# Optimization experiments

Measured on AMD Instinct MI355X. Metric: run time of the kernel, lower is better.

Reference implementation:

```python
import jax, jax.numpy as jnp
import numpy as np

N = 50000      # nodes
E = 600000     # edges
H = 128        # hidden_features (= in_features)
ED = 16        # edge_attr_dim
B = 256        # number of graphs in batch
L = 5          # num_layers
OUT = 128      # out_features


def _xavier(key, shape):
    fan_in, fan_out = shape
    a = float(np.sqrt(6.0 / (fan_in + fan_out)))
    return jax.random.uniform(key, shape, jnp.float32, -a, a)


def setup_inputs() -> dict:
    key = jax.random.key(0)
    ks = jax.random.split(key, 32)
    x = jax.random.normal(ks[0], (N, H), jnp.float32)
    edge_index = jax.random.randint(ks[1], (2, E), 0, N, jnp.int32)
    edge_attr = jax.random.normal(ks[2], (E, ED), jnp.float32)
    batch = jnp.sort(jax.random.randint(ks[3], (N,), 0, B, jnp.int32))
    # per-layer parameters, stacked along leading L axis (in=hidden so uniform)
    node_W = jnp.stack([_xavier(jax.random.fold_in(ks[4], i), (H, H)) for i in range(L)])
    edge_W = jnp.stack([_xavier(jax.random.fold_in(ks[5], i), (ED, H)) for i in range(L)])
    mlp1_W = jnp.stack([_xavier(jax.random.fold_in(ks[6], i), (H, H)) for i in range(L)])
    mlp2_W = jnp.stack([_xavier(jax.random.fold_in(ks[7], i), (H, H)) for i in range(L)])
    zb = jnp.zeros((L, H), jnp.float32)
    # virtual-node update MLP (shared across layers) and final classifier
    vn_w0 = _xavier(ks[8], (H, H)); vn_b0 = jnp.zeros((H,), jnp.float32)
    vn_w1 = _xavier(ks[9], (H, H)); vn_b1 = jnp.zeros((H,), jnp.float32)
    fc_W = _xavier(ks[10], (H, OUT)); fc_b = jnp.zeros((OUT,), jnp.float32)
    vn_init = jnp.zeros((1, H), jnp.float32)  # embedding initialized to 0
    return {
        "x": x, "edge_attr": edge_attr,
        "node_W": node_W, "node_b": zb, "edge_W": edge_W, "edge_b": zb,
        "mlp1_W": mlp1_W, "mlp1_b": zb, "mlp2_W": mlp2_W, "mlp2_b": zb,
        "vn_w0": vn_w0, "vn_b0": vn_b0, "vn_w1": vn_w1, "vn_b1": vn_b1,
        "fc_W": fc_W, "fc_b": fc_b, "vn_init": vn_init,
        "edge_index": edge_index, "batch": batch,
    }


def reference(x, edge_attr, node_W, node_b, edge_W, edge_b, mlp1_W, mlp1_b,
              mlp2_W, mlp2_b, vn_w0, vn_b0, vn_w1, vn_b1, fc_W, fc_b,
              vn_init, edge_index, batch):
    src, dst = edge_index[0], edge_index[1]
    # per-graph node counts for mean pooling (guard against empty graphs)
    counts = jnp.maximum(
        jax.ops.segment_sum(jnp.ones((N, 1), x.dtype), batch, num_segments=B), 1.0)
    vn = jnp.broadcast_to(vn_init, (B, H))  # weight.repeat(batch_size, 1)

    def layer(carry, p):
        xc, vn = carry
        nW, nb, eW, eb, m1W, m1b, m2W, m2b = p
        h = xc @ nW + nb + vn[batch]              # node encode + VN broadcast
        ea = edge_attr @ eW + eb                   # edge encode [E,H]
        msg = h[src] + ea                          # gather + add
        agg = jax.ops.segment_sum(msg, dst, num_segments=N)  # scatter-add
        out = jax.nn.relu(agg @ m1W + m1b) @ m2W + m2b        # layer MLP
        xn = jax.nn.relu(out)
        pooled = jax.ops.segment_sum(xn, batch, num_segments=B) / counts
        vn2 = vn + jax.nn.relu(jax.nn.relu(pooled @ vn_w0 + vn_b0) @ vn_w1 + vn_b1)
        return (xn, vn2), None

    (xf, _), _ = jax.lax.scan(
        layer, (x, vn),
        (node_W, node_b, edge_W, edge_b, mlp1_W, mlp1_b, mlp2_W, mlp2_b))
    pooled = jax.ops.segment_sum(xf, batch, num_segments=B) / counts
    return pooled @ fc_W + fc_b
```

## Files before the change

### kernel.cpp

```cpp
#include <hip/hip_runtime.h>

#define NN 50000
#define EE 600000
#define HH 128
#define EDD 16
#define BB 256
#define LL 5
#define NN16 (NN * 16)
#define NSHADOW 8

typedef float f32x4 __attribute__((ext_vector_type(4)));
typedef _Float16 f16x4 __attribute__((ext_vector_type(4)));
typedef _Float16 f16x8 __attribute__((ext_vector_type(8)));

__global__ __launch_bounds__(256) void wprep_k(const float* __restrict__ W,
    _Float16* __restrict__ Wh, _Float16* __restrict__ Wl, int total)
{
    int idx = blockIdx.x * 256 + threadIdx.x;
    if (idx >= total) return;
    int mat = idx >> 14;
    int r = idx & 16383;
    int j = r & 7, lane = (r >> 3) & 63, ks = (r >> 9) & 3, ntw = (r >> 11) & 7;
    int lm = lane & 15, quad = lane >> 4;
    int n = (ntw >> 1) * 32 + (ntw & 1) * 16 + lm;
    int k = ks * 32 + quad * 8 + j;
    float w = W[(mat << 14) + (k << 7) + n];
    _Float16 h = (_Float16)w;
    Wh[idx] = h;
    Wl[idx] = (_Float16)(w - (float)h);
}

__global__ __launch_bounds__(256) void xprep_k(const float* __restrict__ x,
    _Float16* __restrict__ X)
{
    int i = blockIdx.x * 256 + threadIdx.x;
    if (i >= NN * 32) return;
    float4 v = ((const float4*)x)[i];
    f16x4 o;
    o[0] = (_Float16)v.x; o[1] = (_Float16)v.y; o[2] = (_Float16)v.z; o[3] = (_Float16)v.w;
    ((f16x4*)X)[i] = o;
}

__device__ __forceinline__ void stage_A16(const _Float16* __restrict__ Ag, int M, int brow,
    int tid, _Float16* __restrict__ As)
{
    const int r = tid >> 2, cg = tid & 3;
    const int grow = brow + r;
    _Float16* p = As + r * 136 + cg * 32;
    if (grow < M) {
        const f16x8* s = (const f16x8*)(Ag + (size_t)grow * 128 + cg * 32);
#pragma unroll
        for (int i = 0; i < 4; ++i) ((f16x8*)p)[i] = s[i];
    } else {
        f16x8 z = (f16x8)(_Float16)0;
#pragma unroll
        for (int i = 0; i < 4; ++i) ((f16x8*)p)[i] = z;
    }
}

__device__ __forceinline__ void mfma_stage16(
    const _Float16* __restrict__ As,
    const _Float16* __restrict__ Wh, const _Float16* __restrict__ Wl,
    int wn, int lm, int quad, int lane, f32x4 acc[4][2])
{
    f16x8 Bh[2][4], Bl[2][4];
#pragma unroll
    for (int nt = 0; nt < 2; ++nt)
#pragma unroll
        for (int ks = 0; ks < 4; ++ks) {
            int fi = ((((wn * 2 + nt) * 4) + ks) * 64 + lane) * 8;
            Bh[nt][ks] = *(const f16x8*)(Wh + fi);
            Bl[nt][ks] = *(const f16x8*)(Wl + fi);
        }
#pragma unroll
    for (int ks = 0; ks < 4; ++ks) {
        f16x8 a[4];
#pragma unroll
        for (int mt = 0; mt < 4; ++mt) {
            int off = (mt * 16 + lm) * 136 + ks * 32 + quad * 8;
            a[mt] = *(const f16x8*)(As + off);
        }
#pragma unroll
        for (int mt = 0; mt < 4; ++mt)
#pragma unroll
            for (int nt = 0; nt < 2; ++nt) {
                acc[mt][nt] = __builtin_amdgcn_mfma_f32_16x16x32_f16(a[mt], Bh[nt][ks], acc[mt][nt], 0, 0, 0);
                acc[mt][nt] = __builtin_amdgcn_mfma_f32_16x16x32_f16(a[mt], Bl[nt][ks], acc[mt][nt], 0, 0, 0);
            }
    }
}

__device__ __forceinline__ void store_f16(const _Float16* __restrict__ Fo,
    _Float16* __restrict__ out, int M, int brow, int tid)
{
    const int r = tid >> 2, cg = tid & 3;
    const int grow = brow + r;
    if (grow >= M) return;
    const f16x8* src = (const f16x8*)(Fo + r * 136 + cg * 32);
    f16x8* dst = (f16x8*)(out + (size_t)grow * 128 + cg * 32);
#pragma unroll
    for (int i = 0; i < 4; ++i) dst[i] = src[i];
}

__global__ __launch_bounds__(256) void gemm_fused_k(
    const _Float16* __restrict__ AggX, const _Float16* __restrict__ Extra,
    const _Float16* __restrict__ WNh, const _Float16* __restrict__ WNl,
    const _Float16* __restrict__ W1h, const _Float16* __restrict__ W1l, const float* __restrict__ b1,
    const _Float16* __restrict__ W2h, const _Float16* __restrict__ W2l, const float* __restrict__ b2,
    _Float16* __restrict__ X, float* __restrict__ pooled8,
    const int* __restrict__ batch, int M)
{
    __shared__ __align__(16) _Float16 bufA[64 * 136];
    __shared__ __align__(16) _Float16 bufB[64 * 136];
    const int tid = threadIdx.x, brow = blockIdx.x * 64;

    stage_A16(AggX, M, brow, tid, bufA);
    stage_A16(Extra, M, brow, tid, bufB);
    __syncthreads();

    const int lane = tid & 63, wn = tid >> 6, lm = lane & 15, quad = lane >> 4;
    const int colb = wn * 32 + lm;

    f32x4 acc[4][2];
#pragma unroll
    for (int mt = 0; mt < 4; ++mt) { acc[mt][0] = (f32x4)(0.f); acc[mt][1] = (f32x4)(0.f); }
    mfma_stage16(bufA, WNh, WNl, wn, lm, quad, lane, acc);

#pragma unroll
    for (int mt = 0; mt < 4; ++mt) {
#pragma unroll
        for (int r = 0; r < 4; ++r) {
            int trow = mt * 16 + quad * 4 + r;
            _Float16* p0 = &bufB[trow * 136 + colb];
            _Float16* p1 = &bufB[trow * 136 + colb + 16];
            *p0 = (_Float16)(acc[mt][0][r] + (float)*p0);
            *p1 = (_Float16)(acc[mt][1][r] + (float)*p1);
        }
    }
    __syncthreads();

#pragma unroll
    for (int mt = 0; mt < 4; ++mt) { acc[mt][0] = (f32x4)(0.f); acc[mt][1] = (f32x4)(0.f); }
    mfma_stage16(bufB, W1h, W1l, wn, lm, quad, lane, acc);
    {
        const float c0 = b1[colb], c1 = b1[colb + 16];
#pragma unroll
        for (int mt = 0; mt < 4; ++mt) {
#pragma unroll
            for (int r = 0; r < 4; ++r) {
                int trow = mt * 16 + quad * 4 + r;
                bufA[trow * 136 + colb]      = (_Float16)fmaxf(acc[mt][0][r] + c0, 0.f);
                bufA[trow * 136 + colb + 16] = (_Float16)fmaxf(acc[mt][1][r] + c1, 0.f);
            }
        }
    }
    __syncthreads();

#pragma unroll
    for (int mt = 0; mt < 4; ++mt) { acc[mt][0] = (f32x4)(0.f); acc[mt][1] = (f32x4)(0.f); }
    mfma_stage16(bufA, W2h, W2l, wn, lm, quad, lane, acc);
    {
        const float d0 = b2[colb], d1 = b2[colb + 16];
#pragma unroll
        for (int mt = 0; mt < 4; ++mt) {
#pragma unroll
            for (int r = 0; r < 4; ++r) {
                int trow = mt * 16 + quad * 4 + r;
                bufB[trow * 136 + colb]      = (_Float16)fmaxf(acc[mt][0][r] + d0, 0.f);
                bufB[trow * 136 + colb + 16] = (_Float16)fmaxf(acc[mt][1][r] + d1, 0.f);
            }
        }
    }
    __syncthreads();
    store_f16(bufB, X, M, brow, tid);

    {
        float* pooled = pooled8 + (size_t)(blockIdx.x & (NSHADOW - 1)) * (BB * HH);
        const int c = tid & 127, half = tid >> 7;
        const int row0 = half * 32;
        float sum = 0.f;
        int curg = -1;
        for (int r2 = 0; r2 < 32; ++r2) {
            int grow = brow + row0 + r2;
            if (grow >= M) break;
            int g = batch[grow];
            if (g != curg) {
                if (curg >= 0) atomicAdd(&pooled[curg * 128 + c], sum);
                curg = g; sum = 0.f;
            }
            sum += (float)bufB[(row0 + r2) * 136 + c];
        }
        if (curg >= 0) atomicAdd(&pooled[curg * 128 + c], sum);
    }
}

__global__ __launch_bounds__(256) void aggregate2_k(
    const _Float16* __restrict__ X, const float* __restrict__ aggE,
    const float* __restrict__ eW, const float* __restrict__ eb, const float* __restrict__ nb,
    const _Float16* __restrict__ vn16, int usevn,
    const int* __restrict__ rowstart, const int4* __restrict__ csr,
    _Float16* __restrict__ AggX, _Float16* __restrict__ Extra, int n)
{
    __shared__ float eWs[16 * 128];
    __shared__ float cbs[128];
    const int tid = threadIdx.x;
#pragma unroll
    for (int t = 0; t < 2; ++t) {
        int li = (tid + t * 256) * 4;
        *(float4*)(&eWs[li]) = *(const float4*)(eW + li);
    }
    if (tid < 32) {
        float4 e4 = *(const float4*)(eb + tid * 4);
        float4 n4 = *(const float4*)(nb + tid * 4);
        e4.x += n4.x; e4.y += n4.y; e4.z += n4.z; e4.w += n4.w;
        *(float4*)(&cbs[tid * 4]) = e4;
    }
    __syncthreads();

    const int lane = tid & 15;
    const int node = blockIdx.x * 16 + (tid >> 4);
    if (node >= n) return;
    const int s = rowstart[node], e = rowstart[node + 1];
    const f16x8* X8 = (const f16x8*)X;
    const f16x8* V8 = (const f16x8*)vn16;

    float ax[8], ev[8];
#pragma unroll
    for (int k = 0; k < 8; ++k) { ax[k] = 0.f; ev[k] = 0.f; }

    int p = s;
    for (; p + 4 <= e; p += 4) {
        int4 c0 = csr[p], c1 = csr[p + 1], c2 = csr[p + 2], c3 = csr[p + 3];
        f16x8 x0 = X8[(size_t)c0.x * 16 + lane];
        f16x8 x1 = X8[(size_t)c1.x * 16 + lane];
        f16x8 x2 = X8[(size_t)c2.x * 16 + lane];
        f16x8 x3 = X8[(size_t)c3.x * 16 + lane];
#pragma unroll
        for (int k = 0; k < 8; ++k)
            ax[k] += ((float)x0[k] + (float)x1[k]) + ((float)x2[k] + (float)x3[k]);
        if (usevn) {
            f16x8 v0 = V8[c0.z * 16 + lane];
            f16x8 v1 = V8[c1.z * 16 + lane];
            f16x8 v2 = V8[c2.z * 16 + lane];
            f16x8 v3 = V8[c3.z * 16 + lane];
#pragma unroll
            for (int k = 0; k < 8; ++k)
                ev[k] += ((float)v0[k] + (float)v1[k]) + ((float)v2[k] + (float)v3[k]);
        }
    }
    for (; p < e; ++p) {
        int4 c0 = csr[p];
        f16x8 x0 = X8[(size_t)c0.x * 16 + lane];
#pragma unroll
        for (int k = 0; k < 8; ++k) ax[k] += (float)x0[k];
        if (usevn) {
            f16x8 v0 = V8[c0.z * 16 + lane];
#pragma unroll
            for (int k = 0; k < 8; ++k) ev[k] += (float)v0[k];
        }
    }

    const float degf = (float)(e - s);
    const float* ae = aggE + (size_t)node * 16;
    float et[8];
#pragma unroll
    for (int k = 0; k < 8; ++k) et[k] = ev[k] + degf * cbs[lane * 8 + k];
#pragma unroll
    for (int k = 0; k < 16; ++k) {
        float a = ae[k];
        float4 wa = *(const float4*)(&eWs[k * 128 + lane * 8]);
        float4 wb = *(const float4*)(&eWs[k * 128 + lane * 8 + 4]);
        et[0] = fmaf(a, wa.x, et[0]); et[1] = fmaf(a, wa.y, et[1]);
        et[2] = fmaf(a, wa.z, et[2]); et[3] = fmaf(a, wa.w, et[3]);
        et[4] = fmaf(a, wb.x, et[4]); et[5] = fmaf(a, wb.y, et[5]);
        et[6] = fmaf(a, wb.z, et[6]); et[7] = fmaf(a, wb.w, et[7]);
    }

    f16x8 ox, oe;
#pragma unroll
    for (int k = 0; k < 8; ++k) { ox[k] = (_Float16)ax[k]; oe[k] = (_Float16)et[k]; }
    ((f16x8*)AggX)[(size_t)node * 16 + lane] = ox;
    ((f16x8*)Extra)[(size_t)node * 16 + lane] = oe;
}

__global__ __launch_bounds__(256) void aggE_k(
    const float* __restrict__ eattr, const int* __restrict__ rowstart,
    const int4* __restrict__ csr, float* __restrict__ aggE, int n)
{
    const int lane = threadIdx.x & 15;
    const int node = blockIdx.x * 16 + (threadIdx.x >> 4);
    if (node >= n) return;
    const int s = rowstart[node], e = rowstart[node + 1];
    float acc = 0.f;
    for (int p = s; p < e; ++p)
        acc += eattr[(size_t)csr[p].y * 16 + lane];
    aggE[(size_t)node * 16 + lane] = acc;
}

__global__ __launch_bounds__(128) void vn_update_k(
    float* __restrict__ pooled8, const int* __restrict__ gstart,
    const float* __restrict__ W0, const float* __restrict__ b0,
    const float* __restrict__ W1, const float* __restrict__ b1,
    float* __restrict__ vn, _Float16* __restrict__ vn16)
{
    __shared__ float p[128], q[128];
    const int g = blockIdx.x, t = threadIdx.x;
    float cnt = (float)(gstart[g + 1] - gstart[g]);
    if (cnt < 1.f) cnt = 1.f;
    float sum = 0.f;
#pragma unroll
    for (int s = 0; s < NSHADOW; ++s) {
        float* slot = pooled8 + (size_t)s * (BB * HH) + g * 128 + t;
        sum += *slot;
        *slot = 0.f;
    }
    p[t] = sum / cnt;
    __syncthreads();
    float a0 = b0[t];
    for (int k = 0; k < 128; ++k) a0 = fmaf(p[k], W0[k * 128 + t], a0);
    q[t] = fmaxf(a0, 0.f);
    __syncthreads();
    float a1 = b1[t];
    for (int k = 0; k < 128; ++k) a1 = fmaf(q[k], W1[k * 128 + t], a1);
    float nv = vn[g * 128 + t] + fmaxf(a1, 0.f);
    vn[g * 128 + t] = nv;
    vn16[g * 128 + t] = (_Float16)nv;
}

__global__ __launch_bounds__(128) void fc_k(
    const float* __restrict__ pooled8, const int* __restrict__ gstart,
    const float* __restrict__ W, const float* __restrict__ b,
    float* __restrict__ out)
{
    __shared__ float p[128];
    const int g = blockIdx.x, t = threadIdx.x;
    float cnt = (float)(gstart[g + 1] - gstart[g]);
    if (cnt < 1.f) cnt = 1.f;
    float sum = 0.f;
#pragma unroll
    for (int s = 0; s < NSHADOW; ++s)
        sum += pooled8[(size_t)s * (BB * HH) + g * 128 + t];
    p[t] = sum / cnt;
    __syncthreads();
    float acc = b[t];
    for (int k = 0; k < 128; ++k) acc = fmaf(p[k], W[k * 128 + t], acc);
    out[g * 128 + t] = acc;
}

__global__ void histp_k(const int* __restrict__ idx, int n, int* __restrict__ cntp)
{
    int i = blockIdx.x * 256 + threadIdx.x;
    if (i < n) atomicAdd(&cntp[(blockIdx.x & 3) * NN16 + (idx[i] << 4)], 1);
}

__global__ void scan_deg_k(const int* __restrict__ degp, int n, int* __restrict__ out, int* __restrict__ bsum)
{
    __shared__ int s[256];
    int gid = blockIdx.x * 256 + threadIdx.x;
    int v = 0;
    if (gid < n) {
        int o = gid << 4;
        v = degp[o] + degp[NN16 + o] + degp[2 * NN16 + o] + degp[3 * NN16 + o];
    }
    s[threadIdx.x] = v;
    __syncthreads();
    for (int off = 1; off < 256; off <<= 1) {
        int t = (threadIdx.x >= off) ? s[threadIdx.x - off] : 0;
        __syncthreads();
        s[threadIdx.x] += t;
        __syncthreads();
    }
    int incl = s[threadIdx.x];
    if (gid < n) out[gid] = incl - v;
    if (bsum != nullptr && threadIdx.x == 255) bsum[blockIdx.x] = incl;
}

__global__ void scan_k(const int* __restrict__ in, int n, int* __restrict__ out, int* __restrict__ bsum)
{
    __shared__ int s[256];
    int gid = blockIdx.x * 256 + threadIdx.x;
    int v = (gid < n) ? in[gid] : 0;
    s[threadIdx.x] = v;
    __syncthreads();
    for (int off = 1; off < 256; off <<= 1) {
        int t = (threadIdx.x >= off) ? s[threadIdx.x - off] : 0;
        __syncthreads();
        s[threadIdx.x] += t;
        __syncthreads();
    }
    int incl = s[threadIdx.x];
    if (gid < n) out[gid] = incl - v;
    if (bsum != nullptr && threadIdx.x == 255) bsum[blockIdx.x] = incl;
}

__global__ void addoff_k(int* __restrict__ data, const int* __restrict__ boff, int n, int total)
{
    int i = blockIdx.x * 256 + threadIdx.x;
    if (i < n) data[i] += boff[blockIdx.x];
    if (i == 0) data[n] = total;
}

__global__ void curinit_k(const int* __restrict__ rowstart, int* __restrict__ cursorp)
{
    int i = blockIdx.x * 256 + threadIdx.x;
    if (i < NN) cursorp[i << 4] = rowstart[i];
}

__global__ void fill_k(const int* __restrict__ dst, const int* __restrict__ src, int n,
                       const int* __restrict__ batch,
                       int* __restrict__ cursorp, int4* __restrict__ csr)
{
    int e = blockIdx.x * 256 + threadIdx.x;
    if (e < n) {
        int sv = src[e];
        int slot = atomicAdd(&cursorp[dst[e] << 4], 1);
        int4 pr; pr.x = sv; pr.y = e; pr.z = batch[sv]; pr.w = 0;
        csr[slot] = pr;
    }
}

__global__ void gstart_k(const int* __restrict__ batch, int* __restrict__ gstart)
{
    int b = blockIdx.x * 64 + threadIdx.x;
    if (b > BB) return;
    if (b == BB) { gstart[BB] = NN; return; }
    int lo = 0, hi = NN;
    while (lo < hi) {
        int mid = (lo + hi) >> 1;
        if (batch[mid] < b) lo = mid + 1; else hi = mid;
    }
    gstart[b] = lo;
}

__global__ void vninit_k(const float* __restrict__ vninit, float* __restrict__ vn,
                         _Float16* __restrict__ vn16, float* __restrict__ pooled8)
{
    int i = blockIdx.x * 256 + threadIdx.x;
    if (i < BB * HH) {
        float v = vninit[i & 127];
        vn[i] = v;
        vn16[i] = (_Float16)v;
    }
    if (i < NSHADOW * BB * HH) pooled8[i] = 0.f;
}

extern "C" void kernel_launch(void* const* d_in, const int* in_sizes, int n_in,
                              void* d_out, int out_size, void* d_ws, size_t ws_size,
                              hipStream_t stream)
{
    (void)in_sizes; (void)n_in; (void)out_size; (void)ws_size;
    const float* x       = (const float*)d_in[0];
    const float* eattr   = (const float*)d_in[1];
    const float* node_W  = (const float*)d_in[2];
    const float* node_b  = (const float*)d_in[3];
    const float* edge_W  = (const float*)d_in[4];
    const float* edge_b  = (const float*)d_in[5];
    const float* mlp1_W  = (const float*)d_in[6];
    const float* mlp1_b  = (const float*)d_in[7];
    const float* mlp2_W  = (const float*)d_in[8];
    const float* mlp2_b  = (const float*)d_in[9];
    const float* vn_w0   = (const float*)d_in[10];
    const float* vn_b0   = (const float*)d_in[11];
    const float* vn_w1   = (const float*)d_in[12];
    const float* vn_b1   = (const float*)d_in[13];
    const float* fc_W    = (const float*)d_in[14];
    const float* fc_b    = (const float*)d_in[15];
    const float* vn_init = (const float*)d_in[16];
    const int*   eidx    = (const int*)d_in[17];
    const int*   batch   = (const int*)d_in[18];
    const int* srcv = eidx;
    const int* dstv = eidx + EE;

    char* wp = (char*)d_ws;
    auto alloc = [&](size_t bytes) -> void* {
        void* p = (void*)wp;
        wp += (bytes + 255) & ~(size_t)255;
        return p;
    };
    _Float16* X0   = (_Float16*)alloc((size_t)NN * HH * 2);
    _Float16* X    = (_Float16*)alloc((size_t)NN * HH * 2);
    _Float16* AggX = (_Float16*)alloc((size_t)NN * HH * 2);
    _Float16* Extra= (_Float16*)alloc((size_t)NN * HH * 2);
    float* aggE    = (float*)alloc((size_t)NN * EDD * 4);
    float* vn      = (float*)alloc((size_t)BB * HH * 4);
    _Float16* vn16 = (_Float16*)alloc((size_t)BB * HH * 2);
    float* pooled8 = (float*)alloc((size_t)NSHADOW * BB * HH * 4);
    int* degp      = (int*)alloc((size_t)4 * NN16 * 4);
    int* rowstart  = (int*)alloc((size_t)(NN + 1) * 4);
    int* cursorp   = (int*)alloc((size_t)NN16 * 4);
    int4* csr      = (int4*)alloc((size_t)EE * 16);
    int* bsum      = (int*)alloc(256 * 4);
    int* boff      = (int*)alloc(256 * 4);
    int* gstart    = (int*)alloc((size_t)(BB + 1) * 4);
    _Float16* WtN_h = (_Float16*)alloc((size_t)5 * 16384 * 2);
    _Float16* WtN_l = (_Float16*)alloc((size_t)5 * 16384 * 2);
    _Float16* Wt1_h = (_Float16*)alloc((size_t)5 * 16384 * 2);
    _Float16* Wt1_l = (_Float16*)alloc((size_t)5 * 16384 * 2);
    _Float16* Wt2_h = (_Float16*)alloc((size_t)5 * 16384 * 2);
    _Float16* Wt2_l = (_Float16*)alloc((size_t)5 * 16384 * 2);

    hipMemsetAsync(degp, 0, (size_t)4 * NN16 * 4, stream);

    histp_k<<<(EE + 255) / 256, 256, 0, stream>>>(dstv, EE, degp);

    const int NB1 = (NN + 255) / 256;
    scan_deg_k<<<NB1, 256, 0, stream>>>(degp, NN, rowstart, bsum);
    scan_k<<<1, 256, 0, stream>>>(bsum, NB1, boff, nullptr);
    addoff_k<<<NB1, 256, 0, stream>>>(rowstart, boff, NN, EE);
    curinit_k<<<NB1, 256, 0, stream>>>(rowstart, cursorp);
    fill_k<<<(EE + 255) / 256, 256, 0, stream>>>(dstv, srcv, EE, batch, cursorp, csr);

    gstart_k<<<5, 64, 0, stream>>>(batch, gstart);

    aggE_k<<<(NN + 15) / 16, 256, 0, stream>>>(eattr, rowstart, csr, aggE, NN);
    vninit_k<<<(NSHADOW * BB * HH) / 256, 256, 0, stream>>>(vn_init, vn, vn16, pooled8);
    xprep_k<<<(NN * 32 + 255) / 256, 256, 0, stream>>>(x, X0);

    wprep_k<<<(5 * 16384 + 255) / 256, 256, 0, stream>>>(node_W, WtN_h, WtN_l, 5 * 16384);
    wprep_k<<<(5 * 16384 + 255) / 256, 256, 0, stream>>>(mlp1_W, Wt1_h, Wt1_l, 5 * 16384);
    wprep_k<<<(5 * 16384 + 255) / 256, 256, 0, stream>>>(mlp2_W, Wt2_h, Wt2_l, 5 * 16384);

    const int GN = (NN + 63) / 64;
    const _Float16* xin = X0;
    for (int l = 0; l < LL; ++l) {
        aggregate2_k<<<(NN + 15) / 16, 256, 0, stream>>>(xin, aggE,
            edge_W + (size_t)l * EDD * HH, edge_b + (size_t)l * HH, node_b + (size_t)l * HH,
            vn16, (l > 0) ? 1 : 0, rowstart, csr, AggX, Extra, NN);
        gemm_fused_k<<<GN, 256, 0, stream>>>(AggX, Extra,
            WtN_h + (size_t)l * 16384, WtN_l + (size_t)l * 16384,
            Wt1_h + (size_t)l * 16384, Wt1_l + (size_t)l * 16384, mlp1_b + (size_t)l * HH,
            Wt2_h + (size_t)l * 16384, Wt2_l + (size_t)l * 16384, mlp2_b + (size_t)l * HH,
            X, pooled8, batch, NN);
        if (l < LL - 1)
            vn_update_k<<<BB, 128, 0, stream>>>(pooled8, gstart, vn_w0, vn_b0, vn_w1, vn_b1, vn, vn16);
        xin = X;
    }
    fc_k<<<BB, 128, 0, stream>>>(pooled8, gstart, fc_W, fc_b, (float*)d_out);
}
```

Measured before the change: 624.7 us.

## Fold edge-attr and virtual-node terms into MFMA GEMM via precomputed count matrices

Each layer's per-edge edge-encoding sum and virtual-node gather are rewritten algebraically. The aggregated edge attributes (hi/lo fp16 split plus a degree column) are multiplied by a fused edge weight/bias fragment. A precomputed per-node graph-count matrix C (N x 256) is multiplied by the virtual-node embedding, and both products run on MFMA inside the fused GEMM. The gather kernel now only sums neighbour features using a slimmer int CSR, which cuts per-edge vn loads and the Extra buffer round trip. In exchange it adds a 51MB count histogram with atomics, a 25MB Cfrag buffer read every layer, an extra K=256 MFMA pass, and fp16 rounding of counts and vn.

```diff
diff --git a/kernel.cpp b/kernel.cpp
--- a/kernel.cpp
+++ b/kernel.cpp
@@ -30,6 +30,25 @@
     Wl[idx] = (_Float16)(w - (float)h);
 }
 
+__global__ __launch_bounds__(256) void bext_k(const float* __restrict__ eW,
+    const float* __restrict__ eb, const float* __restrict__ nb,
+    _Float16* __restrict__ BXh, _Float16* __restrict__ BXl)
+{
+    int idx = blockIdx.x * 256 + threadIdx.x;
+    if (idx >= 5 * 8192) return;
+    int j = idx & 7, lane = (idx >> 3) & 63, ks = (idx >> 9) & 1, ntw = (idx >> 10) & 7, l = idx >> 13;
+    int lm = lane & 15, quad = lane >> 4;
+    int n = (ntw >> 1) * 32 + (ntw & 1) * 16 + lm;
+    int k = ks * 32 + quad * 8 + j;
+    float v = 0.f;
+    if (k < 16) v = eW[((size_t)l * 16 + k) * 128 + n];
+    else if (k < 32) v = eW[((size_t)l * 16 + (k - 16)) * 128 + n];
+    else if (k == 32) v = eb[l * 128 + n] + nb[l * 128 + n];
+    _Float16 h = (_Float16)v;
+    BXh[idx] = h;
+    BXl[idx] = (_Float16)(v - (float)h);
+}
+
 __global__ __launch_bounds__(256) void xprep_k(const float* __restrict__ x,
     _Float16* __restrict__ X)
 {
@@ -103,8 +122,10 @@
 }
 
 __global__ __launch_bounds__(256) void gemm_fused_k(
-    const _Float16* __restrict__ AggX, const _Float16* __restrict__ Extra,
+    const _Float16* __restrict__ AggX, const _Float16* __restrict__ Afix,
+    const _Float16* __restrict__ Cfrag, const _Float16* __restrict__ vnB, int usevn,
     const _Float16* __restrict__ WNh, const _Float16* __restrict__ WNl,
+    const _Float16* __restrict__ BXh, const _Float16* __restrict__ BXl,
     const _Float16* __restrict__ W1h, const _Float16* __restrict__ W1l, const float* __restrict__ b1,
     const _Float16* __restrict__ W2h, const _Float16* __restrict__ W2l, const float* __restrict__ b2,
     _Float16* __restrict__ X, float* __restrict__ pooled8,
@@ -115,7 +136,18 @@
     const int tid = threadIdx.x, brow = blockIdx.x * 64;
 
     stage_A16(AggX, M, brow, tid, bufA);
-    stage_A16(Extra, M, brow, tid, bufB);
+    {
+        const int r = tid >> 2, cg = tid & 3;
+        const int grow = brow + r;
+        _Float16* p = bufB + r * 72 + cg * 16;
+        if (grow < M) {
+            const f16x8* s = (const f16x8*)(Afix + (size_t)grow * 64 + cg * 16);
+            ((f16x8*)p)[0] = s[0]; ((f16x8*)p)[1] = s[1];
+        } else {
+            f16x8 z = (f16x8)(_Float16)0;
+            ((f16x8*)p)[0] = z; ((f16x8*)p)[1] = z;
+        }
+    }
     __syncthreads();
 
     const int lane = tid & 63, wn = tid >> 6, lm = lane & 15, quad = lane >> 4;
@@ -124,24 +156,61 @@
     f32x4 acc[4][2];
 #pragma unroll
     for (int mt = 0; mt < 4; ++mt) { acc[mt][0] = (f32x4)(0.f); acc[mt][1] = (f32x4)(0.f); }
+
     mfma_stage16(bufA, WNh, WNl, wn, lm, quad, lane, acc);
+
+#pragma unroll
+    for (int ksf = 0; ksf < 2; ++ksf) {
+        f16x8 Bh[2], Bl[2];
+#pragma unroll
+        for (int nt = 0; nt < 2; ++nt) {
+            int fi = (((wn * 2 + nt) * 2 + ksf) * 64 + lane) * 8;
+            Bh[nt] = *(const f16x8*)(BXh + fi);
+            Bl[nt] = *(const f16x8*)(BXl + fi);
+        }
+#pragma unroll
+        for (int mt = 0; mt < 4; ++mt) {
+            f16x8 a = *(const f16x8*)(bufB + (mt * 16 + lm) * 72 + ksf * 32 + quad * 8);
+#pragma unroll
+            for (int nt = 0; nt < 2; ++nt) {
+                acc[mt][nt] = __builtin_amdgcn_mfma_f32_16x16x32_f16(a, Bh[nt], acc[mt][nt], 0, 0, 0);
+                acc[mt][nt] = __builtin_amdgcn_mfma_f32_16x16x32_f16(a, Bl[nt], acc[mt][nt], 0, 0, 0);
+            }
+        }
+    }
+
+    if (usevn) {
+        const _Float16* Cb = Cfrag + (size_t)blockIdx.x * 16384;
+#pragma unroll
+        for (int ks = 0; ks < 8; ++ks) {
+            f16x8 bv[2];
+#pragma unroll
+            for (int nt = 0; nt < 2; ++nt)
+                bv[nt] = *(const f16x8*)(vnB + (((ks * 8 + (wn * 2 + nt)) * 64 + lane) * 8));
+#pragma unroll
+            for (int mt = 0; mt < 4; ++mt) {
+                f16x8 av = *(const f16x8*)(Cb + (((mt * 8 + ks) * 64 + lane) * 8));
+                acc[mt][0] = __builtin_amdgcn_mfma_f32_16x16x32_f16(av, bv[0], acc[mt][0], 0, 0, 0);
+                acc[mt][1] = __builtin_amdgcn_mfma_f32_16x16x32_f16(av, bv[1], acc[mt][1], 0, 0, 0);
+            }
+        }
+    }
+    __syncthreads();
 
 #pragma unroll
     for (int mt = 0; mt < 4; ++mt) {
 #pragma unroll
         for (int r = 0; r < 4; ++r) {
             int trow = mt * 16 + quad * 4 + r;
-            _Float16* p0 = &bufB[trow * 136 + colb];
-            _Float16* p1 = &bufB[trow * 136 + colb + 16];
-            *p0 = (_Float16)(acc[mt][0][r] + (float)*p0);
-            *p1 = (_Float16)(acc[mt][1][r] + (float)*p1);
+            bufA[trow * 136 + colb]      = (_Float16)acc[mt][0][r];
+            bufA[trow * 136 + colb + 16] = (_Float16)acc[mt][1][r];
         }
     }
     __syncthreads();
 
 #pragma unroll
     for (int mt = 0; mt < 4; ++mt) { acc[mt][0] = (f32x4)(0.f); acc[mt][1] = (f32x4)(0.f); }
-    mfma_stage16(bufB, W1h, W1l, wn, lm, quad, lane, acc);
+    mfma_stage16(bufA, W1h, W1l, wn, lm, quad, lane, acc);
     {
         const float c0 = b1[colb], c1 = b1[colb + 16];
 #pragma unroll
@@ -149,8 +218,8 @@
 #pragma unroll
             for (int r = 0; r < 4; ++r) {
                 int trow = mt * 16 + quad * 4 + r;
-                bufA[trow * 136 + colb]      = (_Float16)fmaxf(acc[mt][0][r] + c0, 0.f);
-                bufA[trow * 136 + colb + 16] = (_Float16)fmaxf(acc[mt][1][r] + c1, 0.f);
+                bufB[trow * 136 + colb]      = (_Float16)fmaxf(acc[mt][0][r] + c0, 0.f);
+                bufB[trow * 136 + colb + 16] = (_Float16)fmaxf(acc[mt][1][r] + c1, 0.f);
             }
         }
     }
@@ -158,7 +227,7 @@
 
 #pragma unroll
     for (int mt = 0; mt < 4; ++mt) { acc[mt][0] = (f32x4)(0.f); acc[mt][1] = (f32x4)(0.f); }
-    mfma_stage16(bufA, W2h, W2l, wn, lm, quad, lane, acc);
+    mfma_stage16(bufB, W2h, W2l, wn, lm, quad, lane, acc);
     {
         const float d0 = b2[colb], d1 = b2[colb + 16];
 #pragma unroll
@@ -166,13 +235,13 @@
 #pragma unroll
             for (int r = 0; r < 4; ++r) {
                 int trow = mt * 16 + quad * 4 + r;
-                bufB[trow * 136 + colb]      = (_Float16)fmaxf(acc[mt][0][r] + d0, 0.f);
-                bufB[trow * 136 + colb + 16] = (_Float16)fmaxf(acc[mt][1][r] + d1, 0.f);
+                bufA[trow * 136 + colb]      = (_Float16)fmaxf(acc[mt][0][r] + d0, 0.f);
+                bufA[trow * 136 + colb + 16] = (_Float16)fmaxf(acc[mt][1][r] + d1, 0.f);
             }
         }
     }
     __syncthreads();
-    store_f16(bufB, X, M, brow, tid);
+    store_f16(bufA, X, M, brow, tid);
 
     {
         float* pooled = pooled8 + (size_t)(blockIdx.x & (NSHADOW - 1)) * (BB * HH);
@@ -188,120 +257,113 @@
                 if (curg >= 0) atomicAdd(&pooled[curg * 128 + c], sum);
                 curg = g; sum = 0.f;
             }
-            sum += (float)bufB[(row0 + r2) * 136 + c];
+            sum += (float)bufA[(row0 + r2) * 136 + c];
         }
         if (curg >= 0) atomicAdd(&pooled[curg * 128 + c], sum);
     }
 }
 
-__global__ __launch_bounds__(256) void aggregate2_k(
-    const _Float16* __restrict__ X, const float* __restrict__ aggE,
-    const float* __restrict__ eW, const float* __restrict__ eb, const float* __restrict__ nb,
-    const _Float16* __restrict__ vn16, int usevn,
-    const int* __restrict__ rowstart, const int4* __restrict__ csr,
-    _Float16* __restrict__ AggX, _Float16* __restrict__ Extra, int n)
-{
-    __shared__ float eWs[16 * 128];
-    __shared__ float cbs[128];
+__global__ __launch_bounds__(256) void gather_k(
+    const _Float16* __restrict__ X, const int* __restrict__ rowstart,
+    const int* __restrict__ csrc, _Float16* __restrict__ AggX, int n)
+{
     const int tid = threadIdx.x;
-#pragma unroll
-    for (int t = 0; t < 2; ++t) {
-        int li = (tid + t * 256) * 4;
-        *(float4*)(&eWs[li]) = *(const float4*)(eW + li);
-    }
-    if (tid < 32) {
-        float4 e4 = *(const float4*)(eb + tid * 4);
-        float4 n4 = *(const float4*)(nb + tid * 4);
-        e4.x += n4.x; e4.y += n4.y; e4.z += n4.z; e4.w += n4.w;
-        *(float4*)(&cbs[tid * 4]) = e4;
-    }
-    __syncthreads();
-
     const int lane = tid & 15;
     const int node = blockIdx.x * 16 + (tid >> 4);
     if (node >= n) return;
     const int s = rowstart[node], e = rowstart[node + 1];
     const f16x8* X8 = (const f16x8*)X;
-    const f16x8* V8 = (const f16x8*)vn16;
-
-    float ax[8], ev[8];
-#pragma unroll
-    for (int k = 0; k < 8; ++k) { ax[k] = 0.f; ev[k] = 0.f; }
+
+    float ax[8];
+#pragma unroll
+    for (int k = 0; k < 8; ++k) ax[k] = 0.f;
 
     int p = s;
     for (; p + 4 <= e; p += 4) {
-        int4 c0 = csr[p], c1 = csr[p + 1], c2 = csr[p + 2], c3 = csr[p + 3];
-        f16x8 x0 = X8[(size_t)c0.x * 16 + lane];
-        f16x8 x1 = X8[(size_t)c1.x * 16 + lane];
-        f16x8 x2 = X8[(size_t)c2.x * 16 + lane];
-        f16x8 x3 = X8[(size_t)c3.x * 16 + lane];
+        int s0 = csrc[p], s1 = csrc[p + 1], s2 = csrc[p + 2], s3 = csrc[p + 3];
+        f16x8 x0 = X8[(size_t)s0 * 16 + lane];
+        f16x8 x1 = X8[(size_t)s1 * 16 + lane];
+        f16x8 x2 = X8[(size_t)s2 * 16 + lane];
+        f16x8 x3 = X8[(size_t)s3 * 16 + lane];
 #pragma unroll
         for (int k = 0; k < 8; ++k)
             ax[k] += ((float)x0[k] + (float)x1[k]) + ((float)x2[k] + (float)x3[k]);
-        if (usevn) {
-            f16x8 v0 = V8[c0.z * 16 + lane];
-            f16x8 v1 = V8[c1.z * 16 + lane];
-            f16x8 v2 = V8[c2.z * 16 + lane];
-            f16x8 v3 = V8[c3.z * 16 + lane];
-#pragma unroll
-            for (int k = 0; k < 8; ++k)
-                ev[k] += ((float)v0[k] + (float)v1[k]) + ((float)v2[k] + (float)v3[k]);
-        }
     }
     for (; p < e; ++p) {
-        int4 c0 = csr[p];
-        f16x8 x0 = X8[(size_t)c0.x * 16 + lane];
+        f16x8 x0 = X8[(size_t)csrc[p] * 16 + lane];
 #pragma unroll
         for (int k = 0; k < 8; ++k) ax[k] += (float)x0[k];
-        if (usevn) {
-            f16x8 v0 = V8[c0.z * 16 + lane];
-#pragma unroll
-            for (int k = 0; k < 8; ++k) ev[k] += (float)v0[k];
-        }
-    }
-
-    const float degf = (float)(e - s);
-    const float* ae = aggE + (size_t)node * 16;
-    float et[8];
-#pragma unroll
-    for (int k = 0; k < 8; ++k) et[k] = ev[k] + degf * cbs[lane * 8 + k];
-#pragma unroll
-    for (int k = 0; k < 16; ++k) {
-        float a = ae[k];
-        float4 wa = *(const float4*)(&eWs[k * 128 + lane * 8]);
-        float4 wb = *(const float4*)(&eWs[k * 128 + lane * 8 + 4]);
-        et[0] = fmaf(a, wa.x, et[0]); et[1] = fmaf(a, wa.y, et[1]);
-        et[2] = fmaf(a, wa.z, et[2]); et[3] = fmaf(a, wa.w, et[3]);
-        et[4] = fmaf(a, wb.x, et[4]); et[5] = fmaf(a, wb.y, et[5]);
-        et[6] = fmaf(a, wb.z, et[6]); et[7] = fmaf(a, wb.w, et[7]);
-    }
-
-    f16x8 ox, oe;
-#pragma unroll
-    for (int k = 0; k < 8; ++k) { ox[k] = (_Float16)ax[k]; oe[k] = (_Float16)et[k]; }
-    ((f16x8*)AggX)[(size_t)node * 16 + lane] = ox;
-    ((f16x8*)Extra)[(size_t)node * 16 + lane] = oe;
-}
-
-__global__ __launch_bounds__(256) void aggE_k(
-    const float* __restrict__ eattr, const int* __restrict__ rowstart,
-    const int4* __restrict__ csr, float* __restrict__ aggE, int n)
-{
-    const int lane = threadIdx.x & 15;
-    const int node = blockIdx.x * 16 + (threadIdx.x >> 4);
+    }
+
+    f16x8 o;
+#pragma unroll
+    for (int k = 0; k < 8; ++k) o[k] = (_Float16)ax[k];
+    ((f16x8*)AggX)[(size_t)node * 16 + lane] = o;
+}
+
+__global__ __launch_bounds__(256) void aggEat_k(
+    const float* __restrict__ eattr, const int* __restrict__ dstv,
+    float* __restrict__ aggE)
+{
+    int i = blockIdx.x * 256 + threadIdx.x;
+    if (i >= EE * 16) return;
+    int e = i >> 4, k = i & 15;
+    atomicAdd(&aggE[(size_t)dstv[e] * 16 + k], eattr[i]);
+}
+
+__global__ __launch_bounds__(256) void afix_k(
+    const float* __restrict__ aggE, const int* __restrict__ rowstart,
+    _Float16* __restrict__ Afix, int n)
+{
+    const int tid = threadIdx.x;
+    const int node = blockIdx.x * 64 + (tid >> 2);
     if (node >= n) return;
-    const int s = rowstart[node], e = rowstart[node + 1];
-    float acc = 0.f;
-    for (int p = s; p < e; ++p)
-        acc += eattr[(size_t)csr[p].y * 16 + lane];
-    aggE[(size_t)node * 16 + lane] = acc;
+    const int cg = tid & 3;
+    _Float16* dst = Afix + (size_t)node * 64 + cg * 16;
+    f16x8 o0 = (f16x8)(_Float16)0, o1 = (f16x8)(_Float16)0;
+    if (cg < 2) {
+        const float* ae = aggE + (size_t)node * 16;
+#pragma unroll
+        for (int k = 0; k < 16; ++k) {
+            float v = ae[k];
+            _Float16 h = (_Float16)v;
+            _Float16 out = (cg == 0) ? h : (_Float16)(v - (float)h);
+            if (k < 8) o0[k] = out; else o1[k - 8] = out;
+        }
+    } else if (cg == 2) {
+        o0[0] = (_Float16)(float)(rowstart[node + 1] - rowstart[node]);
+    }
+    ((f16x8*)dst)[0] = o0;
+    ((f16x8*)dst)[1] = o1;
+}
+
+__global__ void histC_k(const int* __restrict__ dstv, const int* __restrict__ srcv,
+                        const int* __restrict__ batch, int* __restrict__ Cint)
+{
+    int i = blockIdx.x * 256 + threadIdx.x;
+    if (i < EE) atomicAdd(&Cint[(size_t)dstv[i] * 256 + batch[srcv[i]]], 1);
+}
+
+__global__ __launch_bounds__(256) void cfrag_k(const int* __restrict__ Cint,
+                                               _Float16* __restrict__ Cfrag)
+{
+    const int brow = blockIdx.x * 64;
+    const size_t base = (size_t)blockIdx.x * 16384;
+    for (int e = threadIdx.x; e < 16384; e += 256) {
+        int j = e & 7, lane = (e >> 3) & 63, ks = (e >> 9) & 7, mt = e >> 12;
+        int row = brow + mt * 16 + (lane & 15);
+        int g = ks * 32 + (lane >> 4) * 8 + j;
+        _Float16 v = (_Float16)0;
+        if (row < NN) v = (_Float16)(float)Cint[(size_t)row * 256 + g];
+        Cfrag[base + e] = v;
+    }
 }
 
 __global__ __launch_bounds__(128) void vn_update_k(
     float* __restrict__ pooled8, const int* __restrict__ gstart,
     const float* __restrict__ W0, const float* __restrict__ b0,
     const float* __restrict__ W1, const float* __restrict__ b1,
-    float* __restrict__ vn, _Float16* __restrict__ vn16)
+    float* __restrict__ vn, _Float16* __restrict__ vnB)
 {
     __shared__ float p[128], q[128];
     const int g = blockIdx.x, t = threadIdx.x;
@@ -324,7 +386,12 @@
     for (int k = 0; k < 128; ++k) a1 = fmaf(q[k], W1[k * 128 + t], a1);
     float nv = vn[g * 128 + t] + fmaxf(a1, 0.f);
     vn[g * 128 + t] = nv;
-    vn16[g * 128 + t] = (_Float16)nv;
+    {
+        int ks = g >> 5, quad = (g >> 3) & 3, j = g & 7;
+        int tt = ((t >> 5) << 1) | ((t >> 4) & 1);
+        int lanev = quad * 16 + (t & 15);
+        vnB[((ks * 8 + tt) * 64 + lanev) * 8 + j] = (_Float16)nv;
+    }
 }
 
 __global__ __launch_bounds__(128) void fc_k(
@@ -393,29 +460,25 @@
     if (bsum != nullptr && threadIdx.x == 255) bsum[blockIdx.x] = incl;
 }
 
-__global__ void addoff_k(int* __restrict__ data, const int* __restrict__ boff, int n, int total)
+__global__ void addoff_k(int* __restrict__ data, const int* __restrict__ boff,
+                         int* __restrict__ cursorp, int n, int total)
 {
     int i = blockIdx.x * 256 + threadIdx.x;
-    if (i < n) data[i] += boff[blockIdx.x];
+    if (i < n) {
+        int v = data[i] + boff[blockIdx.x];
+        data[i] = v;
+        cursorp[i << 4] = v;
+    }
     if (i == 0) data[n] = total;
 }
 
-__global__ void curinit_k(const int* __restrict__ rowstart, int* __restrict__ cursorp)
-{
-    int i = blockIdx.x * 256 + threadIdx.x;
-    if (i < NN) cursorp[i << 4] = rowstart[i];
-}
-
 __global__ void fill_k(const int* __restrict__ dst, const int* __restrict__ src, int n,
-                       const int* __restrict__ batch,
-                       int* __restrict__ cursorp, int4* __restrict__ csr)
+                       int* __restrict__ cursorp, int* __restrict__ csrc)
 {
     int e = blockIdx.x * 256 + threadIdx.x;
     if (e < n) {
-        int sv = src[e];
         int slot = atomicAdd(&cursorp[dst[e] << 4], 1);
-        int4 pr; pr.x = sv; pr.y = e; pr.z = batch[sv]; pr.w = 0;
-        csr[slot] = pr;
+        csrc[slot] = src[e];
     }
 }
 
@@ -433,13 +496,12 @@
 }
 
 __global__ void vninit_k(const float* __restrict__ vninit, float* __restrict__ vn,
-                         _Float16* __restrict__ vn16, float* __restrict__ pooled8)
+                         _Float16* __restrict__ vnB, float* __restrict__ pooled8)
 {
     int i = blockIdx.x * 256 + threadIdx.x;
     if (i < BB * HH) {
-        float v = vninit[i & 127];
-        vn[i] = v;
-        vn16[i] = (_Float16)v;
+        vn[i] = vninit[i & 127];
+        vnB[i] = (_Float16)0;
     }
     if (i < NSHADOW * BB * HH) pooled8[i] = 0.f;
 }
@@ -477,18 +539,22 @@
         wp += (bytes + 255) & ~(size_t)255;
         return p;
     };
+    int* degp      = (int*)alloc((size_t)4 * NN16 * 4);
+    int* Cint      = (int*)alloc((size_t)NN * BB * 4);
+    float* aggE    = (float*)alloc((size_t)NN * EDD * 4);
+    const size_t zero_bytes = (size_t)4 * NN16 * 4 + (size_t)NN * BB * 4 + (size_t)NN * EDD * 4;
+
     _Float16* X0   = (_Float16*)alloc((size_t)NN * HH * 2);
     _Float16* X    = (_Float16*)alloc((size_t)NN * HH * 2);
     _Float16* AggX = (_Float16*)alloc((size_t)NN * HH * 2);
-    _Float16* Extra= (_Float16*)alloc((size_t)NN * HH * 2);
-    float* aggE    = (float*)alloc((size_t)NN * EDD * 4);
+    _Float16* Afix = (_Float16*)alloc((size_t)NN * 64 * 2);
+    _Float16* Cfrag= (_Float16*)alloc((size_t)782 * 16384 * 2);
     float* vn      = (float*)alloc((size_t)BB * HH * 4);
-    _Float16* vn16 = (_Float16*)alloc((size_t)BB * HH * 2);
+    _Float16* vnB  = (_Float16*)alloc((size_t)BB * HH * 2);
     float* pooled8 = (float*)alloc((size_t)NSHADOW * BB * HH * 4);
-    int* degp      = (int*)alloc((size_t)4 * NN16 * 4);
     int* rowstart  = (int*)alloc((size_t)(NN + 1) * 4);
     int* cursorp   = (int*)alloc((size_t)NN16 * 4);
-    int4* csr      = (int4*)alloc((size_t)EE * 16);
+    int* csrc      = (int*)alloc((size_t)EE * 4);
     int* bsum      = (int*)alloc(256 * 4);
     int* boff      = (int*)alloc(256 * 4);
     int* gstart    = (int*)alloc((size_t)(BB + 1) * 4);
@@ -498,41 +564,45 @@
     _Float16* Wt1_l = (_Float16*)alloc((size_t)5 * 16384 * 2);
     _Float16* Wt2_h = (_Float16*)alloc((size_t)5 * 16384 * 2);
     _Float16* Wt2_l = (_Float16*)alloc((size_t)5 * 16384 * 2);
-
-    hipMemsetAsync(degp, 0, (size_t)4 * NN16 * 4, stream);
+    _Float16* BXh   = (_Float16*)alloc((size_t)5 * 8192 * 2);
+    _Float16* BXl   = (_Float16*)alloc((size_t)5 * 8192 * 2);
+
+    hipMemsetAsync(degp, 0, zero_bytes, stream);
 
     histp_k<<<(EE + 255) / 256, 256, 0, stream>>>(dstv, EE, degp);
+    histC_k<<<(EE + 255) / 256, 256, 0, stream>>>(dstv, srcv, batch, Cint);
+    aggEat_k<<<(EE * 16 + 255) / 256, 256, 0, stream>>>(eattr, dstv, aggE);
 
     const int NB1 = (NN + 255) / 256;
     scan_deg_k<<<NB1, 256, 0, stream>>>(degp, NN, rowstart, bsum);
     scan_k<<<1, 256, 0, stream>>>(bsum, NB1, boff, nullptr);
-    addoff_k<<<NB1, 256, 0, stream>>>(rowstart, boff, NN, EE);
-    curinit_k<<<NB1, 256, 0, stream>>>(rowstart, cursorp);
-    fill_k<<<(EE + 255) / 256, 256, 0, stream>>>(dstv, srcv, EE, batch, cursorp, csr);
+    addoff_k<<<NB1, 256, 0, stream>>>(rowstart, boff, cursorp, NN, EE);
+    fill_k<<<(EE + 255) / 256, 256, 0, stream>>>(dstv, srcv, EE, cursorp, csrc);
 
     gstart_k<<<5, 64, 0, stream>>>(batch, gstart);
 
-    aggE_k<<<(NN + 15) / 16, 256, 0, stream>>>(eattr, rowstart, csr, aggE, NN);
-    vninit_k<<<(NSHADOW * BB * HH) / 256, 256, 0, stream>>>(vn_init, vn, vn16, pooled8);
+    afix_k<<<(NN + 63) / 64, 256, 0, stream>>>(aggE, rowstart, Afix, NN);
+    cfrag_k<<<(NN + 63) / 64, 256, 0, stream>>>(Cint, Cfrag);
+    vninit_k<<<(NSHADOW * BB * HH) / 256, 256, 0, stream>>>(vn_init, vn, vnB, pooled8);
     xprep_k<<<(NN * 32 + 255) / 256, 256, 0, stream>>>(x, X0);
 
     wprep_k<<<(5 * 16384 + 255) / 256, 256, 0, stream>>>(node_W, WtN_h, WtN_l, 5 * 16384);
     wprep_k<<<(5 * 16384 + 255) / 256, 256, 0, stream>>>(mlp1_W, Wt1_h, Wt1_l, 5 * 16384);
     wprep_k<<<(5 * 16384 + 255) / 256, 256, 0, stream>>>(mlp2_W, Wt2_h, Wt2_l, 5 * 16384);
+    bext_k<<<(5 * 8192 + 255) / 256, 256, 0, stream>>>(edge_W, edge_b, node_b, BXh, BXl);
 
     const int GN = (NN + 63) / 64;
     const _Float16* xin = X0;
     for (int l = 0; l < LL; ++l) {
-        aggregate2_k<<<(NN + 15) / 16, 256, 0, stream>>>(xin, aggE,
-            edge_W + (size_t)l * EDD * HH, edge_b + (size_t)l * HH, node_b + (size_t)l * HH,
-            vn16, (l > 0) ? 1 : 0, rowstart, csr, AggX, Extra, NN);
-        gemm_fused_k<<<GN, 256, 0, stream>>>(AggX, Extra,
+        gather_k<<<(NN + 15) / 16, 256, 0, stream>>>(xin, rowstart, csrc, AggX, NN);
+        gemm_fused_k<<<GN, 256, 0, stream>>>(AggX, Afix, Cfrag, vnB, (l > 0) ? 1 : 0,
             WtN_h + (size_t)l * 16384, WtN_l + (size_t)l * 16384,
+            BXh + (size_t)l * 8192, BXl + (size_t)l * 8192,
             Wt1_h + (size_t)l * 16384, Wt1_l + (size_t)l * 16384, mlp1_b + (size_t)l * HH,
             Wt2_h + (size_t)l * 16384, Wt2_l + (size_t)l * 16384, mlp2_b + (size_t)l * HH,
             X, pooled8, batch, NN);
         if (l < LL - 1)
-            vn_update_k<<<BB, 128, 0, stream>>>(pooled8, gstart, vn_w0, vn_b0, vn_w1, vn_b1, vn, vn16);
+            vn_update_k<<<BB, 128, 0, stream>>>(pooled8, gstart, vn_w0, vn_b0, vn_w1, vn_b1, vn, vnB);
         xin = X;
     }
     fc_k<<<BB, 128, 0, stream>>>(pooled8, gstart, fc_W, fc_b, (float*)d_out);
```

After: 607.9 us. 2.7% less time.
